# Kernel optimization log

Hardware: AMD Instinct MI355X
Metric: run time of the kernel (lower is better)

Reference implementation:

```python
import jax, jax.numpy as jnp
import numpy as np

L = 2          # num_hidden_layers
B, S, H = 2, 2048, 1024
NH, DH = 16, 64   # heads, head dim
FF = 4096
EPS = 1e-5


def setup_inputs() -> dict:
    key = jax.random.key(0)
    ks = jax.random.split(key, 20)
    s = 0.02
    inp = {
        "hidden_states": jax.random.normal(ks[0], (B, S, H), jnp.float32),
        "attention_mask": jnp.zeros((B, 1, 1, S), jnp.float32),
        "Wq": jax.random.normal(ks[1], (L, H, H), jnp.float32) * s,
        "bq": jnp.zeros((L, H), jnp.float32),
        "Wk": jax.random.normal(ks[2], (L, H, H), jnp.float32) * s,
        "bk": jnp.zeros((L, H), jnp.float32),
        "Wv": jax.random.normal(ks[3], (L, H, H), jnp.float32) * s,
        "bv": jnp.zeros((L, H), jnp.float32),
        "Wao": jax.random.normal(ks[4], (L, H, H), jnp.float32) * s,
        "bao": jnp.zeros((L, H), jnp.float32),
        "ln1_g": jnp.ones((L, H), jnp.float32),
        "ln1_b": jnp.zeros((L, H), jnp.float32),
        "Wi": jax.random.normal(ks[5], (L, H, FF), jnp.float32) * s,
        "bi": jnp.zeros((L, FF), jnp.float32),
        "Wo": jax.random.normal(ks[6], (L, FF, H), jnp.float32) * s,
        "bo": jnp.zeros((L, H), jnp.float32),
        "ln2_g": jnp.ones((L, H), jnp.float32),
        "ln2_b": jnp.zeros((L, H), jnp.float32),
    }
    return inp


def _layernorm(x, g, b):
    m = jnp.mean(x, axis=-1, keepdims=True)
    v = jnp.var(x, axis=-1, keepdims=True)
    return (x - m) * jax.lax.rsqrt(v + EPS) * g + b


def _split_heads(x):
    # [B,S,H] -> [B,NH,S,DH]
    return x.reshape(B, S, NH, DH).transpose(0, 2, 1, 3)


def _layer(x, mask, Wq, bq, Wk, bk, Wv, bv, Wao, bao, g1, b1, Wi, bi, Wo, bo, g2, b2):
    q = _split_heads(x @ Wq + bq)
    k = _split_heads(x @ Wk + bk)
    v = _split_heads(x @ Wv + bv)
    scores = jnp.einsum('bhqd,bhkd->bhqk', q, k) / np.sqrt(DH).astype(np.float32)
    scores = scores + mask  # additive attention mask
    probs = jax.nn.softmax(scores, axis=-1)
    ctx = jnp.einsum('bhqk,bhkd->bhqd', probs, v)
    ctx = ctx.transpose(0, 2, 1, 3).reshape(B, S, H)
    x = _layernorm(ctx @ Wao + bao + x, g1, b1)
    ffn = jax.nn.gelu(x @ Wi + bi, approximate=False) @ Wo + bo
    return _layernorm(ffn + x, g2, b2)


def reference(hidden_states, attention_mask, Wq, bq, Wk, bk, Wv, bv, Wao, bao,
              ln1_g, ln1_b, Wi, bi, Wo, bo, ln2_g, ln2_b):
    x = hidden_states
    for i in range(L):
        x = _layer(x, attention_mask,
                   Wq[i], bq[i], Wk[i], bk[i], Wv[i], bv[i], Wao[i], bao[i],
                   ln1_g[i], ln1_b[i], Wi[i], bi[i], Wo[i], bo[i], ln2_g[i], ln2_b[i])
    return x
```

## Files before the change

kernel.cpp:

```cpp
#include <hip/hip_runtime.h>

typedef _Float16 half_t;
typedef _Float16 half8  __attribute__((ext_vector_type(8)));
typedef _Float16 half4v __attribute__((ext_vector_type(4)));
typedef float    f32x4  __attribute__((ext_vector_type(4)));

#define AS1 __attribute__((address_space(1)))
#define AS3 __attribute__((address_space(3)))

#define MODE_H16  0
#define MODE_F32R 1
#define MODE_GELU 2

__device__ __forceinline__ f32x4 zero4() {
    f32x4 z; z[0] = 0.f; z[1] = 0.f; z[2] = 0.f; z[3] = 0.f; return z;
}

__device__ __forceinline__ half8 lds_frag(const half_t* p) {
    union { uint4 u; half8 h; } c;
    c.u = *(const uint4*)p;
    return c.h;
}

__device__ __forceinline__ float gelu_f(float v) {
    float t = v * v;
    float u = v * (1.595769122f + 0.0713548163f * t);
    return v / (1.f + __expf(-u));
}

__device__ __forceinline__ void gl_lds16(const half_t* g, half_t* l) {
    __builtin_amdgcn_global_load_lds(
        (AS1 unsigned int*)(unsigned long long)(const void*)g,
        (AS3 unsigned int*)l,
        16, 0, 0);
}


__global__ __launch_bounds__(256) void gemm_bt(
    const half_t* __restrict__ A,
    const half_t* __restrict__ Bt,
    const float*  __restrict__ bias,
    const float*  __restrict__ res,
    void* __restrict__ out,
    int M, int N, int K, int mode)
{
    __shared__ __align__(16) half_t As[128 * 64];
    __shared__ __align__(16) half_t Bs[128 * 64];

    const int tid  = threadIdx.x;
    const int w    = tid >> 6, lane = tid & 63;
    const int m0   = blockIdx.y * 128, n0 = blockIdx.x * 128;
    const int g    = lane >> 4, ml = lane & 15, m7 = ml & 7;
    const int mo   = (w >> 1) * 64, no = (w & 1) * 64;
    const int r8   = lane >> 3;
    const int sck  = ((lane & 7) ^ (r8 & 7)) * 8;

    f32x4 acc[4][4];
#pragma unroll
    for (int i = 0; i < 4; i++)
#pragma unroll
        for (int j = 0; j < 4; j++) acc[i][j] = zero4();

    const half_t* Ag = A  + (size_t)m0 * K;
    const half_t* Bg = Bt + (size_t)n0 * K;

    for (int k0 = 0; k0 < K; k0 += 64) {
        __syncthreads();
#pragma unroll
        for (int i = 0; i < 4; i++) {
            int t = w * 4 + i;
            gl_lds16(Ag + (size_t)(t * 8 + r8) * K + k0 + sck, &As[t * 512]);
            gl_lds16(Bg + (size_t)(t * 8 + r8) * K + k0 + sck, &Bs[t * 512]);
        }
        __syncthreads();
#pragma unroll
        for (int kk = 0; kk < 2; kk++) {
            const int co = ((kk * 4 + g) ^ m7) * 8;
            half8 af[4], bf[4];
#pragma unroll
            for (int i = 0; i < 4; i++) af[i] = lds_frag(&As[(mo + i * 16 + ml) * 64 + co]);
#pragma unroll
            for (int j = 0; j < 4; j++) bf[j] = lds_frag(&Bs[(no + j * 16 + ml) * 64 + co]);
#pragma unroll
            for (int i = 0; i < 4; i++)
#pragma unroll
                for (int j = 0; j < 4; j++)
                    acc[i][j] = __builtin_amdgcn_mfma_f32_16x16x32_f16(af[i], bf[j], acc[i][j], 0, 0, 0);
        }
    }

    const int gm0 = m0 + mo, gn0 = n0 + no;
#pragma unroll
    for (int j = 0; j < 4; j++) {
        int col = gn0 + j * 16 + ml;
        float bv = bias[col];
#pragma unroll
        for (int i = 0; i < 4; i++) {
#pragma unroll
            for (int r = 0; r < 4; r++) {
                int row = gm0 + i * 16 + g * 4 + r;
                float v = acc[i][j][r] + bv;
                size_t idx = (size_t)row * N + col;
                if (mode == MODE_F32R) {
                    ((float*)out)[idx] = v + res[idx];
                } else if (mode == MODE_GELU) {
                    ((half_t*)out)[idx] = (half_t)gelu_f(v);
                } else {
                    ((half_t*)out)[idx] = (half_t)v;
                }
            }
        }
    }
}

__global__ __launch_bounds__(256) void gemm_bt64(
    const half_t* __restrict__ A,
    const half_t* __restrict__ Bt,
    const float*  __restrict__ bias,
    const float*  __restrict__ res,
    float* __restrict__ out,
    int M, int N, int K)
{
    __shared__ __align__(16) half_t As[128 * 64];
    __shared__ __align__(16) half_t Bs[64 * 64];

    const int tid  = threadIdx.x;
    const int w    = tid >> 6, lane = tid & 63;
    const int m0   = blockIdx.y * 128, n0 = blockIdx.x * 64;
    const int g    = lane >> 4, ml = lane & 15, m7 = ml & 7;
    const int mo   = w * 32;
    const int r8   = lane >> 3;
    const int sck  = ((lane & 7) ^ (r8 & 7)) * 8;

    f32x4 acc[2][4];
#pragma unroll
    for (int i = 0; i < 2; i++)
#pragma unroll
        for (int j = 0; j < 4; j++) acc[i][j] = zero4();

    const half_t* Ag = A  + (size_t)m0 * K;
    const half_t* Bg = Bt + (size_t)n0 * K;

    for (int k0 = 0; k0 < K; k0 += 64) {
        __syncthreads();
#pragma unroll
        for (int i = 0; i < 4; i++) {
            int t = w * 4 + i;
            gl_lds16(Ag + (size_t)(t * 8 + r8) * K + k0 + sck, &As[t * 512]);
        }
#pragma unroll
        for (int i = 0; i < 2; i++) {
            int t = w * 2 + i;
            gl_lds16(Bg + (size_t)(t * 8 + r8) * K + k0 + sck, &Bs[t * 512]);
        }
        __syncthreads();
#pragma unroll
        for (int kk = 0; kk < 2; kk++) {
            const int co = ((kk * 4 + g) ^ m7) * 8;
            half8 af[2], bf[4];
#pragma unroll
            for (int i = 0; i < 2; i++) af[i] = lds_frag(&As[(mo + i * 16 + ml) * 64 + co]);
#pragma unroll
            for (int j = 0; j < 4; j++) bf[j] = lds_frag(&Bs[(j * 16 + ml) * 64 + co]);
#pragma unroll
            for (int i = 0; i < 2; i++)
#pragma unroll
                for (int j = 0; j < 4; j++)
                    acc[i][j] = __builtin_amdgcn_mfma_f32_16x16x32_f16(af[i], bf[j], acc[i][j], 0, 0, 0);
        }
    }

    const int gm0 = m0 + mo;
#pragma unroll
    for (int j = 0; j < 4; j++) {
        int col = n0 + j * 16 + ml;
        float bv = bias[col];
#pragma unroll
        for (int i = 0; i < 2; i++) {
#pragma unroll
            for (int r = 0; r < 4; r++) {
                int row = gm0 + i * 16 + g * 4 + r;
                size_t idx = (size_t)row * N + col;
                out[idx] = acc[i][j][r] + bv + res[idx];
            }
        }
    }
}

__global__ __launch_bounds__(256) void gemm_qkv(
    const half_t* __restrict__ A,
    const half_t* __restrict__ Bt,
    const float*  __restrict__ bq,
    const float*  __restrict__ bk,
    const float*  __restrict__ bv,
    half_t* __restrict__ Qo, half_t* __restrict__ Ko, half_t* __restrict__ Vto,
    int M, int K)
{
    __shared__ __align__(16) half_t As[128 * 64];
    __shared__ __align__(16) half_t Bs[128 * 64];

    const int tid  = threadIdx.x;
    const int w    = tid >> 6, lane = tid & 63;
    const int m0   = blockIdx.y * 128, n0 = blockIdx.x * 128;
    const int g    = lane >> 4, ml = lane & 15, m7 = ml & 7;
    const int mo   = (w >> 1) * 64, no = (w & 1) * 64;
    const int r8   = lane >> 3;
    const int sck  = ((lane & 7) ^ (r8 & 7)) * 8;

    f32x4 acc[4][4];
#pragma unroll
    for (int i = 0; i < 4; i++)
#pragma unroll
        for (int j = 0; j < 4; j++) acc[i][j] = zero4();

    const half_t* Ag = A  + (size_t)m0 * K;
    const half_t* Bg = Bt + (size_t)n0 * K;

    for (int k0 = 0; k0 < K; k0 += 64) {
        __syncthreads();
#pragma unroll
        for (int i = 0; i < 4; i++) {
            int t = w * 4 + i;
            gl_lds16(Ag + (size_t)(t * 8 + r8) * K + k0 + sck, &As[t * 512]);
            gl_lds16(Bg + (size_t)(t * 8 + r8) * K + k0 + sck, &Bs[t * 512]);
        }
        __syncthreads();
#pragma unroll
        for (int kk = 0; kk < 2; kk++) {
            const int co = ((kk * 4 + g) ^ m7) * 8;
            half8 af[4], bf[4];
#pragma unroll
            for (int i = 0; i < 4; i++) af[i] = lds_frag(&As[(mo + i * 16 + ml) * 64 + co]);
#pragma unroll
            for (int j = 0; j < 4; j++) bf[j] = lds_frag(&Bs[(no + j * 16 + ml) * 64 + co]);
#pragma unroll
            for (int i = 0; i < 4; i++)
#pragma unroll
                for (int j = 0; j < 4; j++)
                    acc[i][j] = __builtin_amdgcn_mfma_f32_16x16x32_f16(af[i], bf[j], acc[i][j], 0, 0, 0);
        }
    }

    const int seg  = n0 >> 10;
    const int nloc = (n0 & 1023) + no;
    const float* bias = (seg == 0) ? bq : (seg == 1) ? bk : bv;
    const int gm0 = m0 + mo;

    if (seg < 2) {
        half_t* O = (seg == 0) ? Qo : Ko;
#pragma unroll
        for (int j = 0; j < 4; j++) {
            int col = nloc + j * 16 + ml;
            float bvv = bias[col];
#pragma unroll
            for (int i = 0; i < 4; i++)
#pragma unroll
                for (int r = 0; r < 4; r++)
                    O[(size_t)(gm0 + i * 16 + g * 4 + r) * 1024 + col] =
                        (half_t)(acc[i][j][r] + bvv);
        }
    } else {
#pragma unroll
        for (int j = 0; j < 4; j++) {
            int col = nloc + j * 16 + ml;
            float bvv = bias[col];
#pragma unroll
            for (int i = 0; i < 4; i++) {
                int rowb = gm0 + i * 16 + g * 4;
                int bb = rowb >> 11, sl = rowb & 2047;
                half4v v;
#pragma unroll
                for (int r = 0; r < 4; r++) v[r] = (half_t)(acc[i][j][r] + bvv);
                *(half4v*)&Vto[((size_t)bb * 1024 + col) * 2048 + sl] = v;
            }
        }
    }
}

__global__ __launch_bounds__(256, 4) void flash_attn(
    const half_t* __restrict__ Q,
    const half_t* __restrict__ Kq,
    const half_t* __restrict__ Vt,
    const float*  __restrict__ mask,
    half_t* __restrict__ opart,
    float2* __restrict__ mlpart,
    int S, int H)
{
    __shared__ __align__(16) half_t Ks[64 * 64];
    __shared__ __align__(16) half_t Vs[64 * 64];
    __shared__ __align__(16) half_t Ps[4 * 32 * 64];

    const int qt = blockIdx.x, h = blockIdx.y, z = blockIdx.z;
    const int b = z >> 1, hf = z & 1;
    const int tid = threadIdx.x, w = tid >> 6, lane = tid & 63;
    const int g = lane >> 4, ml = lane & 15, m7 = ml & 7;
    const int NHloc = gridDim.y;
    const int BNHS = 2 * NHloc * S;

    const int q0 = qt * 128 + w * 32;
    const half_t* Qg = Q  + ((size_t)(b * S + q0)) * H + h * 64;
    const half_t* Kg = Kq + ((size_t)b * S) * H + h * 64;
    const half_t* Vg = Vt + ((size_t)b * H + h * 64) * (size_t)S;
    const float*  mk = mask + (size_t)b * S;

    half8 qf[2][2];
#pragma unroll
    for (int qi = 0; qi < 2; qi++)
#pragma unroll
        for (int kk = 0; kk < 2; kk++)
            qf[qi][kk] = *(const half8*)(Qg + (size_t)(qi * 16 + ml) * H + kk * 32 + g * 8);

    float m_[2] = {-1e30f, -1e30f}, l_[2] = {0.f, 0.f};
    f32x4 o[2][4];
#pragma unroll
    for (int qi = 0; qi < 2; qi++)
#pragma unroll
        for (int df = 0; df < 4; df++) o[qi][df] = zero4();

    half_t* Pw = &Ps[w * 32 * 64];
    const int srow = tid >> 3;
    const int sc   = tid & 7;

    const int kvbeg = hf * (S >> 1), kvend = kvbeg + (S >> 1);
    for (int kv0 = kvbeg; kv0 < kvend; kv0 += 64) {
        __syncthreads();
#pragma unroll
        for (int t = 0; t < 2; t++) {
            int row = t * 32 + srow;
            int ck  = sc ^ (row & 7);
            gl_lds16(Kg + (size_t)(kv0 + row) * H + ck * 8, &Ks[(t * 256 + w * 64) * 8]);
            gl_lds16(Vg + (size_t)row * S + kv0 + ck * 8,   &Vs[(t * 256 + w * 64) * 8]);
        }
        __syncthreads();

        f32x4 s[2][4];
#pragma unroll
        for (int kvf = 0; kvf < 4; kvf++) {
            half8 k0 = lds_frag(&Ks[(kvf * 16 + ml) * 64 + ((0 + g) ^ m7) * 8]);
            half8 k1 = lds_frag(&Ks[(kvf * 16 + ml) * 64 + ((4 + g) ^ m7) * 8]);
            s[0][kvf] = __builtin_amdgcn_mfma_f32_16x16x32_f16(k0, qf[0][0], zero4(), 0, 0, 0);
            s[0][kvf] = __builtin_amdgcn_mfma_f32_16x16x32_f16(k1, qf[0][1], s[0][kvf], 0, 0, 0);
            s[1][kvf] = __builtin_amdgcn_mfma_f32_16x16x32_f16(k0, qf[1][0], zero4(), 0, 0, 0);
            s[1][kvf] = __builtin_amdgcn_mfma_f32_16x16x32_f16(k1, qf[1][1], s[1][kvf], 0, 0, 0);
        }
#pragma unroll
        for (int kvf = 0; kvf < 4; kvf++) {
            float4 mv = *(const float4*)(mk + kv0 + kvf * 16 + g * 4);
#pragma unroll
            for (int qi = 0; qi < 2; qi++) {
                s[qi][kvf][0] = s[qi][kvf][0] * 0.125f + mv.x;
                s[qi][kvf][1] = s[qi][kvf][1] * 0.125f + mv.y;
                s[qi][kvf][2] = s[qi][kvf][2] * 0.125f + mv.z;
                s[qi][kvf][3] = s[qi][kvf][3] * 0.125f + mv.w;
            }
        }
        float alpha[2];
#pragma unroll
        for (int qi = 0; qi < 2; qi++) {
            float mx = -1e30f;
#pragma unroll
            for (int kvf = 0; kvf < 4; kvf++)
#pragma unroll
                for (int r = 0; r < 4; r++) mx = fmaxf(mx, s[qi][kvf][r]);
            mx = fmaxf(mx, __shfl_xor(mx, 16));
            mx = fmaxf(mx, __shfl_xor(mx, 32));
            float mnew = fmaxf(m_[qi], mx);
            alpha[qi]  = __expf(m_[qi] - mnew);
            m_[qi] = mnew;
            float ps = 0.f;
#pragma unroll
            for (int kvf = 0; kvf < 4; kvf++)
#pragma unroll
                for (int r = 0; r < 4; r++) {
                    float pv = __expf(s[qi][kvf][r] - mnew);
                    s[qi][kvf][r] = pv; ps += pv;
                }
            ps += __shfl_xor(ps, 16);
            ps += __shfl_xor(ps, 32);
            l_[qi] = l_[qi] * alpha[qi] + ps;
#pragma unroll
            for (int kvf = 0; kvf < 4; kvf++) {
                half4v pk;
#pragma unroll
                for (int r = 0; r < 4; r++) pk[r] = (half_t)s[qi][kvf][r];
                *(half4v*)(Pw + (qi * 16 + ml) * 64 +
                           (((kvf * 2 + (g >> 1)) ^ m7) * 8) + (g & 1) * 4) = pk;
            }
        }
#pragma unroll
        for (int qi = 0; qi < 2; qi++) {
#pragma unroll
            for (int r = 0; r < 4; r++) {
                float a = __shfl(alpha[qi], (lane & 48) + g * 4 + r);
#pragma unroll
                for (int df = 0; df < 4; df++) o[qi][df][r] *= a;
            }
        }
#pragma unroll
        for (int kk = 0; kk < 2; kk++) {
            half8 pa0 = lds_frag(&Pw[(ml)      * 64 + ((kk * 4 + g) ^ m7) * 8]);
            half8 pa1 = lds_frag(&Pw[(16 + ml) * 64 + ((kk * 4 + g) ^ m7) * 8]);
#pragma unroll
            for (int df = 0; df < 4; df++) {
                half8 vb = lds_frag(&Vs[(df * 16 + ml) * 64 + ((kk * 4 + g) ^ m7) * 8]);
                o[0][df] = __builtin_amdgcn_mfma_f32_16x16x32_f16(pa0, vb, o[0][df], 0, 0, 0);
                o[1][df] = __builtin_amdgcn_mfma_f32_16x16x32_f16(pa1, vb, o[1][df], 0, 0, 0);
            }
        }
    }

    const size_t rowbase = (size_t)hf * BNHS + ((size_t)(b * NHloc + h)) * S + q0;
#pragma unroll
    for (int qi = 0; qi < 2; qi++) {
#pragma unroll
        for (int r = 0; r < 4; r++) {
            size_t ro = (rowbase + qi * 16 + g * 4 + r) * 64;
#pragma unroll
            for (int df = 0; df < 4; df++)
                opart[ro + df * 16 + ml] = (half_t)o[qi][df][r];
        }
    }
    if (g == 0) {
#pragma unroll
        for (int qi = 0; qi < 2; qi++)
            mlpart[rowbase + qi * 16 + ml] = make_float2(m_[qi], l_[qi]);
    }
}

__global__ __launch_bounds__(256) void flash_merge(
    const half_t* __restrict__ opart,
    const float2* __restrict__ mlpart,
    half_t* __restrict__ ctx)
{
    int gid = blockIdx.x * 256 + threadIdx.x;
    int row = gid >> 4, dg = (gid & 15) * 4;
    float2 a = mlpart[row], c = mlpart[65536 + row];
    float m  = fmaxf(a.x, c.x);
    float w1 = __expf(a.x - m), w2 = __expf(c.x - m);
    float inv = 1.f / (w1 * a.y + w2 * c.y);
    half4v o1 = *(const half4v*)&opart[(size_t)row * 64 + dg];
    half4v o2 = *(const half4v*)&opart[(size_t)(65536 + row) * 64 + dg];
    int b = row >> 15, hq = row & 32767;
    int h = hq >> 11, q = hq & 2047;
    half4v o;
#pragma unroll
    for (int i = 0; i < 4; i++)
        o[i] = (half_t)((w1 * (float)o1[i] + w2 * (float)o2[i]) * inv);
    *(half4v*)&ctx[((size_t)(b * 2048 + q)) * 1024 + h * 64 + dg] = o;
}

__global__ __launch_bounds__(256) void transpose_cast(
    const float* __restrict__ W, half_t* __restrict__ Wt, int Kd, int Nd)
{
    __shared__ float tile[32][33];
    size_t zoff = (size_t)blockIdx.z * Kd * Nd;
    const float* Wz = W + zoff;
    half_t* Wtz = Wt + zoff;
    int n0 = blockIdx.x * 32, k0 = blockIdx.y * 32;
    int tx = threadIdx.x & 31, ty = threadIdx.x >> 5;
#pragma unroll
    for (int j = 0; j < 4; j++)
        tile[ty + j * 8][tx] = Wz[(size_t)(k0 + ty + j * 8) * Nd + n0 + tx];
    __syncthreads();
#pragma unroll
    for (int j = 0; j < 4; j++)
        Wtz[(size_t)(n0 + ty + j * 8) * Kd + k0 + tx] = (half_t)tile[tx][ty + j * 8];
}

__global__ __launch_bounds__(256) void transpose_qkv(
    const float* __restrict__ Wq, const float* __restrict__ Wk,
    const float* __restrict__ Wv, half_t* __restrict__ WT)
{
    __shared__ float tile[32][33];
    int z = blockIdx.z, l = z / 3, which = z % 3;
    const float* W = ((which == 0) ? Wq : (which == 1) ? Wk : Wv) + (size_t)l * 1024 * 1024;
    half_t* D = WT + ((size_t)l * 3 + which) * 1024 * 1024;
    int n0 = blockIdx.x * 32, k0 = blockIdx.y * 32;
    int tx = threadIdx.x & 31, ty = threadIdx.x >> 5;
#pragma unroll
    for (int j = 0; j < 4; j++)
        tile[ty + j * 8][tx] = W[(size_t)(k0 + ty + j * 8) * 1024 + n0 + tx];
    __syncthreads();
#pragma unroll
    for (int j = 0; j < 4; j++)
        D[(size_t)(n0 + ty + j * 8) * 1024 + k0 + tx] = (half_t)tile[tx][ty + j * 8];
}

__global__ __launch_bounds__(256) void cast_f32_f16(
    const float* __restrict__ in, half_t* __restrict__ out)
{
    int i = blockIdx.x * 256 + threadIdx.x;
    float4 v = ((const float4*)in)[i];
    half4v o; o[0] = (half_t)v.x; o[1] = (half_t)v.y; o[2] = (half_t)v.z; o[3] = (half_t)v.w;
    *(half4v*)(out + (size_t)i * 4) = o;
}

__global__ __launch_bounds__(256) void layernorm_k(
    const float* __restrict__ in,
    const float* __restrict__ gam, const float* __restrict__ bet,
    float* __restrict__ outf, half_t* __restrict__ outh)
{
    int row = blockIdx.x, tid = threadIdx.x;
    const float4 v = ((const float4*)(in + (size_t)row * 1024))[tid];
    float s = v.x + v.y + v.z + v.w;
    float q = v.x * v.x + v.y * v.y + v.z * v.z + v.w * v.w;
    for (int off = 32; off; off >>= 1) { s += __shfl_down(s, off); q += __shfl_down(q, off); }
    __shared__ float ss[4], sq[4];
    int w = tid >> 6;
    if ((tid & 63) == 0) { ss[w] = s; sq[w] = q; }
    __syncthreads();
    float S_ = ss[0] + ss[1] + ss[2] + ss[3];
    float Q_ = sq[0] + sq[1] + sq[2] + sq[3];
    float mean = S_ * (1.f / 1024.f);
    float var  = Q_ * (1.f / 1024.f) - mean * mean;
    float rstd = rsqrtf(var + 1e-5f);
    float4 gm = ((const float4*)gam)[tid];
    float4 bt = ((const float4*)bet)[tid];
    float y0 = (v.x - mean) * rstd * gm.x + bt.x;
    float y1 = (v.y - mean) * rstd * gm.y + bt.y;
    float y2 = (v.z - mean) * rstd * gm.z + bt.z;
    float y3 = (v.w - mean) * rstd * gm.w + bt.w;
    ((float4*)(outf + (size_t)row * 1024))[tid] = make_float4(y0, y1, y2, y3);
    half4v oh; oh[0] = (half_t)y0; oh[1] = (half_t)y1; oh[2] = (half_t)y2; oh[3] = (half_t)y3;
    *(half4v*)(outh + (size_t)row * 1024 + tid * 4) = oh;
}

extern "C" void kernel_launch(void* const* d_in, const int* in_sizes, int n_in,
                              void* d_out, int out_size, void* d_ws, size_t ws_size,
                              hipStream_t stream)
{
    const int Lc = 2, Bb = 2, S = 2048, Hh = 1024, NH = 16, FF = 4096;
    const int M = Bb * S;

    const float* hs   = (const float*)d_in[0];
    const float* mask = (const float*)d_in[1];
    const float* Wq   = (const float*)d_in[2];  const float* bq  = (const float*)d_in[3];
    const float* Wk   = (const float*)d_in[4];  const float* bk  = (const float*)d_in[5];
    const float* Wv   = (const float*)d_in[6];  const float* bv  = (const float*)d_in[7];
    const float* Wao  = (const float*)d_in[8];  const float* bao = (const float*)d_in[9];
    const float* g1   = (const float*)d_in[10]; const float* b1  = (const float*)d_in[11];
    const float* Wi   = (const float*)d_in[12]; const float* bi  = (const float*)d_in[13];
    const float* Wo   = (const float*)d_in[14]; const float* bo  = (const float*)d_in[15];
    const float* g2   = (const float*)d_in[16]; const float* b2  = (const float*)d_in[17];

    char* p = (char*)d_ws;
    auto take = [&](size_t bytes) { char* r = p; p += (bytes + 255) & ~(size_t)255; return r; };

    half_t* WqkvT = (half_t*)take((size_t)Lc * 3 * Hh * Hh * 2);
    half_t* WaoT  = (half_t*)take((size_t)Lc * Hh * Hh * 2);
    half_t* WiT   = (half_t*)take((size_t)Lc * Hh * FF * 2);
    half_t* WoT   = (half_t*)take((size_t)Lc * FF * Hh * 2);
    half_t* xb    = (half_t*)take((size_t)M * Hh * 2);
    half_t* Qb    = (half_t*)take((size_t)M * Hh * 2);
    half_t* Kb2   = (half_t*)take((size_t)M * Hh * 2);
    half_t* Vtb   = (half_t*)take((size_t)M * Hh * 2);
    (void)          take((size_t)M * Hh * 2);
    half_t* h1    = Qb;
    float*  t0    = (float*)take((size_t)M * Hh * 4);
    float*  x1f   = (float*)take((size_t)M * Hh * 4);
    half_t* x1b   = (half_t*)take((size_t)M * Hh * 2);

    half_t* opart  = (half_t*)t0;
    float2* mlpart = (float2*)x1b;

    dim3 tb(256);

    transpose_qkv<<<dim3(32, 32, Lc * 3), tb, 0, stream>>>(Wq, Wk, Wv, WqkvT);
    transpose_cast<<<dim3(32, 32, Lc), tb, 0, stream>>>(Wao, WaoT, Hh, Hh);
    transpose_cast<<<dim3(FF / 32, 32, Lc), tb, 0, stream>>>(Wi, WiT, Hh, FF);
    transpose_cast<<<dim3(32, FF / 32, Lc), tb, 0, stream>>>(Wo, WoT, FF, Hh);
    cast_f32_f16<<<dim3(M * Hh / 1024), tb, 0, stream>>>(hs, xb);

    const float* xres = hs;
    for (int l = 0; l < Lc; l++) {
        const half_t* WqkvTl = WqkvT + (size_t)l * 3 * Hh * Hh;
        const half_t* WaoTl  = WaoT  + (size_t)l * Hh * Hh;
        const half_t* WiTl   = WiT   + (size_t)l * Hh * FF;
        const half_t* WoTl   = WoT   + (size_t)l * FF * Hh;

        gemm_qkv<<<dim3(3072 / 128, M / 128), tb, 0, stream>>>(
            xb, WqkvTl, bq + l * Hh, bk + l * Hh, bv + l * Hh, Qb, Kb2, Vtb, M, Hh);

        flash_attn<<<dim3(S / 128, NH, Bb * 2), tb, 0, stream>>>(
            Qb, Kb2, Vtb, mask, opart, mlpart, S, Hh);
        flash_merge<<<dim3(Bb * NH * S * 16 / 256), tb, 0, stream>>>(opart, mlpart, xb);

        gemm_bt64<<<dim3(Hh / 64, M / 128), tb, 0, stream>>>(
            xb, WaoTl, bao + l * Hh, xres, t0, M, Hh, Hh);
        layernorm_k<<<dim3(M), tb, 0, stream>>>(t0, g1 + l * Hh, b1 + l * Hh, x1f, x1b);

        gemm_bt<<<dim3(FF / 128, M / 128), tb, 0, stream>>>(
            x1b, WiTl, bi + l * FF, nullptr, h1, M, FF, Hh, MODE_GELU);
        gemm_bt64<<<dim3(Hh / 64, M / 128), tb, 0, stream>>>(
            h1, WoTl, bo + l * Hh, x1f, t0, M, Hh, FF);

        float* outf = (l == Lc - 1) ? (float*)d_out : x1f;
        layernorm_k<<<dim3(M), tb, 0, stream>>>(t0, g2 + l * Hh, b2 + l * Hh, outf, xb);
        xres = x1f;
    }
}
```

Baseline: 723.2 us.

## Use 256x256 double-buffered ping-pong MFMA GEMM for QKV and FFN-up

Replaces the 128x128, 256-thread QKV and FFN-up GEMMs with a 256x256-tile, 512-thread kernel. It double-buffers LDS and splits each K-step into four MFMA quadrants, issuing global-to-LDS prefetches for the next tile between them. It also uses s_setprio and barriers to interleave memory and MFMA work. The aim is to raise data reuse per tile and hide load latency behind compute. The cost is 128KB of LDS per block and fewer blocks: 192 for QKV, fewer than the CU count, which may leave CUs idle.

Measured after the change: 683.4 us. 5.5% less time.

```diff
diff --git a/kernel.cpp b/kernel.cpp
--- a/kernel.cpp
+++ b/kernel.cpp
@@ -36,7 +36,122 @@
 }
 
 
-__global__ __launch_bounds__(256) void gemm_bt(
+
+__device__ __forceinline__ void stage_half(
+    const half_t* __restrict__ G, half_t* L, int K, int srow, int sck, int w)
+{
+    gl_lds16(G + (size_t)srow * K + sck,        L + w * 512);
+    gl_lds16(G + (size_t)(64 + srow) * K + sck, L + 4096 + w * 512);
+}
+
+#define LDA(MH)                                                              \
+    _Pragma("unroll")                                                        \
+    for (int m = 0; m < 4; m++) {                                            \
+        af[m][0] = lds_frag(&Ad[abase + (MH) * 4096 + m * 1024 + c0]);       \
+        af[m][1] = lds_frag(&Ad[abase + (MH) * 4096 + m * 1024 + c1]);       \
+    }
+
+#define LDB(NH)                                                              \
+    _Pragma("unroll")                                                        \
+    for (int n = 0; n < 2; n++) {                                            \
+        bf[NH][n][0] = lds_frag(&Bd[bbase + (NH) * 2048 + n * 1024 + c0]);   \
+        bf[NH][n][1] = lds_frag(&Bd[bbase + (NH) * 2048 + n * 1024 + c1]);   \
+    }
+
+#define MFMA_Q(MH, NH)                                                       \
+    _Pragma("unroll")                                                        \
+    for (int m = 0; m < 4; m++)                                              \
+        _Pragma("unroll")                                                    \
+        for (int n = 0; n < 2; n++) {                                        \
+            acc[(MH)*4 + m][(NH)*2 + n] =                                    \
+                __builtin_amdgcn_mfma_f32_16x16x32_f16(                      \
+                    af[m][0], bf[NH][n][0], acc[(MH)*4 + m][(NH)*2 + n],     \
+                    0, 0, 0);                                                \
+            acc[(MH)*4 + m][(NH)*2 + n] =                                    \
+                __builtin_amdgcn_mfma_f32_16x16x32_f16(                      \
+                    af[m][1], bf[NH][n][1], acc[(MH)*4 + m][(NH)*2 + n],     \
+                    0, 0, 0);                                                \
+        }
+
+__device__ __forceinline__ void mfma_core256(
+    const half_t* __restrict__ Ag, const half_t* __restrict__ Bg, int K,
+    half_t* As, half_t* Bs, f32x4 (&acc)[8][4])
+{
+    const int tid  = threadIdx.x;
+    const int w    = tid >> 6, lane = tid & 63;
+    const int wm   = w >> 2, wn = w & 3;
+    const int g    = lane >> 4, ml = lane & 15, m7 = ml & 7;
+    const int srow = tid >> 3;
+    const int sck  = ((tid & 7) ^ (srow & 7)) * 8;
+
+#pragma unroll
+    for (int i = 0; i < 8; i++)
+#pragma unroll
+        for (int j = 0; j < 4; j++) acc[i][j] = zero4();
+
+    const int abase = (wm * 128 + ml) * 64;
+    const int bbase = (wn * 64 + ml) * 64;
+    const int c0 = (g ^ m7) * 8, c1 = ((4 + g) ^ m7) * 8;
+
+    stage_half(Ag, As, K, srow, sck, w);
+    stage_half(Ag + (size_t)128 * K, As + 8192, K, srow, sck, w);
+    stage_half(Bg, Bs, K, srow, sck, w);
+    stage_half(Bg + (size_t)128 * K, Bs + 8192, K, srow, sck, w);
+    asm volatile("s_waitcnt vmcnt(0)" ::: "memory");
+    __builtin_amdgcn_s_barrier();
+
+    const int NT = K >> 6;
+    half8 af[4][2];
+    half8 bf[2][2][2];
+
+    for (int t = 0; t < NT; ++t) {
+        half_t* Ad = As + (t & 1) * 16384;
+        half_t* Bd = Bs + (t & 1) * 16384;
+        half_t* An = As + ((t + 1) & 1) * 16384;
+        half_t* Bn = Bs + ((t + 1) & 1) * 16384;
+        const half_t* Agn = Ag + (t + 1) * 64;
+        const half_t* Bgn = Bg + (t + 1) * 64;
+        const bool pf = (t + 1 < NT);
+
+        LDA(0)
+        LDB(0)
+        if (pf) {
+            stage_half(Agn, An, K, srow, sck, w);
+            stage_half(Agn + (size_t)128 * K, An + 8192, K, srow, sck, w);
+        }
+        __builtin_amdgcn_s_barrier();
+        __builtin_amdgcn_s_setprio(1);
+        MFMA_Q(0, 0)
+        __builtin_amdgcn_s_setprio(0);
+        __builtin_amdgcn_s_barrier();
+
+        LDB(1)
+        if (pf) {
+            stage_half(Bgn, Bn, K, srow, sck, w);
+            stage_half(Bgn + (size_t)128 * K, Bn + 8192, K, srow, sck, w);
+        }
+        __builtin_amdgcn_s_barrier();
+        __builtin_amdgcn_s_setprio(1);
+        MFMA_Q(0, 1)
+        __builtin_amdgcn_s_setprio(0);
+        __builtin_amdgcn_s_barrier();
+
+        LDA(1)
+        __builtin_amdgcn_s_barrier();
+        __builtin_amdgcn_s_setprio(1);
+        MFMA_Q(1, 1)
+        __builtin_amdgcn_s_setprio(0);
+        __builtin_amdgcn_s_barrier();
+
+        __builtin_amdgcn_s_setprio(1);
+        MFMA_Q(1, 0)
+        __builtin_amdgcn_s_setprio(0);
+        asm volatile("s_waitcnt vmcnt(0)" ::: "memory");
+        __builtin_amdgcn_s_barrier();
+    }
+}
+
+__global__ __launch_bounds__(512, 2) void gemm256_bt(
     const half_t* __restrict__ A,
     const half_t* __restrict__ Bt,
     const float*  __restrict__ bias,
@@ -44,62 +159,29 @@
     void* __restrict__ out,
     int M, int N, int K, int mode)
 {
-    __shared__ __align__(16) half_t As[128 * 64];
-    __shared__ __align__(16) half_t Bs[128 * 64];
-
-    const int tid  = threadIdx.x;
-    const int w    = tid >> 6, lane = tid & 63;
-    const int m0   = blockIdx.y * 128, n0 = blockIdx.x * 128;
-    const int g    = lane >> 4, ml = lane & 15, m7 = ml & 7;
-    const int mo   = (w >> 1) * 64, no = (w & 1) * 64;
-    const int r8   = lane >> 3;
-    const int sck  = ((lane & 7) ^ (r8 & 7)) * 8;
-
-    f32x4 acc[4][4];
-#pragma unroll
-    for (int i = 0; i < 4; i++)
-#pragma unroll
-        for (int j = 0; j < 4; j++) acc[i][j] = zero4();
-
-    const half_t* Ag = A  + (size_t)m0 * K;
-    const half_t* Bg = Bt + (size_t)n0 * K;
-
-    for (int k0 = 0; k0 < K; k0 += 64) {
-        __syncthreads();
-#pragma unroll
-        for (int i = 0; i < 4; i++) {
-            int t = w * 4 + i;
-            gl_lds16(Ag + (size_t)(t * 8 + r8) * K + k0 + sck, &As[t * 512]);
-            gl_lds16(Bg + (size_t)(t * 8 + r8) * K + k0 + sck, &Bs[t * 512]);
-        }
-        __syncthreads();
-#pragma unroll
-        for (int kk = 0; kk < 2; kk++) {
-            const int co = ((kk * 4 + g) ^ m7) * 8;
-            half8 af[4], bf[4];
-#pragma unroll
-            for (int i = 0; i < 4; i++) af[i] = lds_frag(&As[(mo + i * 16 + ml) * 64 + co]);
-#pragma unroll
-            for (int j = 0; j < 4; j++) bf[j] = lds_frag(&Bs[(no + j * 16 + ml) * 64 + co]);
-#pragma unroll
-            for (int i = 0; i < 4; i++)
-#pragma unroll
-                for (int j = 0; j < 4; j++)
-                    acc[i][j] = __builtin_amdgcn_mfma_f32_16x16x32_f16(af[i], bf[j], acc[i][j], 0, 0, 0);
-        }
-    }
-
-    const int gm0 = m0 + mo, gn0 = n0 + no;
-#pragma unroll
-    for (int j = 0; j < 4; j++) {
-        int col = gn0 + j * 16 + ml;
+    __shared__ __align__(16) half_t As[2 * 16384];
+    __shared__ __align__(16) half_t Bs[2 * 16384];
+
+    const int m0 = blockIdx.y * 256, n0 = blockIdx.x * 256;
+    f32x4 acc[8][4];
+    mfma_core256(A + (size_t)m0 * K, Bt + (size_t)n0 * K, K, As, Bs, acc);
+
+    const int tid = threadIdx.x;
+    const int w   = tid >> 6, lane = tid & 63;
+    const int wm  = w >> 2, wn = w & 3;
+    const int g   = lane >> 4, ml = lane & 15;
+    const int gm0 = m0 + wm * 128, gn0 = n0 + wn * 64;
+
+#pragma unroll
+    for (int nj = 0; nj < 4; nj++) {
+        int col = gn0 + nj * 16 + ml;
         float bv = bias[col];
 #pragma unroll
-        for (int i = 0; i < 4; i++) {
+        for (int mi = 0; mi < 8; mi++) {
 #pragma unroll
             for (int r = 0; r < 4; r++) {
-                int row = gm0 + i * 16 + g * 4 + r;
-                float v = acc[i][j][r] + bv;
+                int row = gm0 + mi * 16 + g * 4 + r;
+                float v = acc[mi][nj][r] + bv;
                 size_t idx = (size_t)row * N + col;
                 if (mode == MODE_F32R) {
                     ((float*)out)[idx] = v + res[idx];
@@ -113,6 +195,63 @@
     }
 }
 
+__global__ __launch_bounds__(512, 2) void gemm256_qkv(
+    const half_t* __restrict__ A,
+    const half_t* __restrict__ Bt,
+    const float*  __restrict__ bq,
+    const float*  __restrict__ bk,
+    const float*  __restrict__ bv,
+    half_t* __restrict__ Qo, half_t* __restrict__ Ko, half_t* __restrict__ Vto,
+    int M, int K)
+{
+    __shared__ __align__(16) half_t As[2 * 16384];
+    __shared__ __align__(16) half_t Bs[2 * 16384];
+
+    const int m0 = blockIdx.y * 256, n0 = blockIdx.x * 256;
+    f32x4 acc[8][4];
+    mfma_core256(A + (size_t)m0 * K, Bt + (size_t)n0 * K, K, As, Bs, acc);
+
+    const int tid = threadIdx.x;
+    const int w   = tid >> 6, lane = tid & 63;
+    const int wm  = w >> 2, wn = w & 3;
+    const int g   = lane >> 4, ml = lane & 15;
+
+    const int seg   = n0 >> 10;
+    const int nbase = (n0 & 1023) + wn * 64;
+    const float* bias = (seg == 0) ? bq : (seg == 1) ? bk : bv;
+    const int gm0 = m0 + wm * 128;
+
+    if (seg < 2) {
+        half_t* O = (seg == 0) ? Qo : Ko;
+#pragma unroll
+        for (int nj = 0; nj < 4; nj++) {
+            int col = nbase + nj * 16 + ml;
+            float bvv = bias[col];
+#pragma unroll
+            for (int mi = 0; mi < 8; mi++)
+#pragma unroll
+                for (int r = 0; r < 4; r++)
+                    O[(size_t)(gm0 + mi * 16 + g * 4 + r) * 1024 + col] =
+                        (half_t)(acc[mi][nj][r] + bvv);
+        }
+    } else {
+#pragma unroll
+        for (int nj = 0; nj < 4; nj++) {
+            int col = nbase + nj * 16 + ml;
+            float bvv = bias[col];
+#pragma unroll
+            for (int mi = 0; mi < 8; mi++) {
+                int rowb = gm0 + mi * 16 + g * 4;
+                int bb = rowb >> 11, sl = rowb & 2047;
+                half4v v4;
+#pragma unroll
+                for (int r = 0; r < 4; r++) v4[r] = (half_t)(acc[mi][nj][r] + bvv);
+                *(half4v*)&Vto[((size_t)bb * 1024 + col) * 2048 + sl] = v4;
+            }
+        }
+    }
+}
+
 __global__ __launch_bounds__(256) void gemm_bt64(
     const half_t* __restrict__ A,
     const half_t* __restrict__ Bt,
@@ -182,96 +321,6 @@
                 int row = gm0 + i * 16 + g * 4 + r;
                 size_t idx = (size_t)row * N + col;
                 out[idx] = acc[i][j][r] + bv + res[idx];
-            }
-        }
-    }
-}
-
-__global__ __launch_bounds__(256) void gemm_qkv(
-    const half_t* __restrict__ A,
-    const half_t* __restrict__ Bt,
-    const float*  __restrict__ bq,
-    const float*  __restrict__ bk,
-    const float*  __restrict__ bv,
-    half_t* __restrict__ Qo, half_t* __restrict__ Ko, half_t* __restrict__ Vto,
-    int M, int K)
-{
-    __shared__ __align__(16) half_t As[128 * 64];
-    __shared__ __align__(16) half_t Bs[128 * 64];
-
-    const int tid  = threadIdx.x;
-    const int w    = tid >> 6, lane = tid & 63;
-    const int m0   = blockIdx.y * 128, n0 = blockIdx.x * 128;
-    const int g    = lane >> 4, ml = lane & 15, m7 = ml & 7;
-    const int mo   = (w >> 1) * 64, no = (w & 1) * 64;
-    const int r8   = lane >> 3;
-    const int sck  = ((lane & 7) ^ (r8 & 7)) * 8;
-
-    f32x4 acc[4][4];
-#pragma unroll
-    for (int i = 0; i < 4; i++)
-#pragma unroll
-        for (int j = 0; j < 4; j++) acc[i][j] = zero4();
-
-    const half_t* Ag = A  + (size_t)m0 * K;
-    const half_t* Bg = Bt + (size_t)n0 * K;
-
-    for (int k0 = 0; k0 < K; k0 += 64) {
-        __syncthreads();
-#pragma unroll
-        for (int i = 0; i < 4; i++) {
-            int t = w * 4 + i;
-            gl_lds16(Ag + (size_t)(t * 8 + r8) * K + k0 + sck, &As[t * 512]);
-            gl_lds16(Bg + (size_t)(t * 8 + r8) * K + k0 + sck, &Bs[t * 512]);
-        }
-        __syncthreads();
-#pragma unroll
-        for (int kk = 0; kk < 2; kk++) {
-            const int co = ((kk * 4 + g) ^ m7) * 8;
-            half8 af[4], bf[4];
-#pragma unroll
-            for (int i = 0; i < 4; i++) af[i] = lds_frag(&As[(mo + i * 16 + ml) * 64 + co]);
-#pragma unroll
-            for (int j = 0; j < 4; j++) bf[j] = lds_frag(&Bs[(no + j * 16 + ml) * 64 + co]);
-#pragma unroll
-            for (int i = 0; i < 4; i++)
-#pragma unroll
-                for (int j = 0; j < 4; j++)
-                    acc[i][j] = __builtin_amdgcn_mfma_f32_16x16x32_f16(af[i], bf[j], acc[i][j], 0, 0, 0);
-        }
-    }
-
-    const int seg  = n0 >> 10;
-    const int nloc = (n0 & 1023) + no;
-    const float* bias = (seg == 0) ? bq : (seg == 1) ? bk : bv;
-    const int gm0 = m0 + mo;
-
-    if (seg < 2) {
-        half_t* O = (seg == 0) ? Qo : Ko;
-#pragma unroll
-        for (int j = 0; j < 4; j++) {
-            int col = nloc + j * 16 + ml;
-            float bvv = bias[col];
-#pragma unroll
-            for (int i = 0; i < 4; i++)
-#pragma unroll
-                for (int r = 0; r < 4; r++)
-                    O[(size_t)(gm0 + i * 16 + g * 4 + r) * 1024 + col] =
-                        (half_t)(acc[i][j][r] + bvv);
-        }
-    } else {
-#pragma unroll
-        for (int j = 0; j < 4; j++) {
-            int col = nloc + j * 16 + ml;
-            float bvv = bias[col];
-#pragma unroll
-            for (int i = 0; i < 4; i++) {
-                int rowb = gm0 + i * 16 + g * 4;
-                int bb = rowb >> 11, sl = rowb & 2047;
-                half4v v;
-#pragma unroll
-                for (int r = 0; r < 4; r++) v[r] = (half_t)(acc[i][j][r] + bvv);
-                *(half4v*)&Vto[((size_t)bb * 1024 + col) * 2048 + sl] = v;
             }
         }
     }
@@ -578,7 +627,7 @@
         const half_t* WiTl   = WiT   + (size_t)l * Hh * FF;
         const half_t* WoTl   = WoT   + (size_t)l * FF * Hh;
 
-        gemm_qkv<<<dim3(3072 / 128, M / 128), tb, 0, stream>>>(
+        gemm256_qkv<<<dim3(3072 / 256, M / 256), dim3(512), 0, stream>>>(
             xb, WqkvTl, bq + l * Hh, bk + l * Hh, bv + l * Hh, Qb, Kb2, Vtb, M, Hh);
 
         flash_attn<<<dim3(S / 128, NH, Bb * 2), tb, 0, stream>>>(
@@ -589,7 +638,7 @@
             xb, WaoTl, bao + l * Hh, xres, t0, M, Hh, Hh);
         layernorm_k<<<dim3(M), tb, 0, stream>>>(t0, g1 + l * Hh, b1 + l * Hh, x1f, x1b);
 
-        gemm_bt<<<dim3(FF / 128, M / 128), tb, 0, stream>>>(
+        gemm256_bt<<<dim3(FF / 256, M / 256), dim3(512), 0, stream>>>(
             x1b, WiTl, bi + l * FF, nullptr, h1, M, FF, Hh, MODE_GELU);
         gemm_bt64<<<dim3(Hh / 64, M / 128), tb, 0, stream>>>(
             h1, WoTl, bo + l * Hh, x1f, t0, M, Hh, FF);
```
